# Optimization experiments

Hardware: AMD Instinct MI355X
Metric: run time of the kernel (lower is better)

## Reference

```python
import jax, jax.numpy as jnp
import numpy as np

B, N, I = 8, 1024, 64
E, H, D = 2, 2, 128   # edge types, heads per layer, hidden dim
O = 64                # num_outputs
IN1 = E * H * D       # layer-1 filter input dim (concat of layer-0 heads)


def setup_inputs() -> dict:
    key = jax.random.key(0)
    ks = jax.random.split(key, 20)
    s = lambda f: 1.0 / np.sqrt(f)
    inp = {
        "nodes": jax.random.normal(ks[0], (B, N, I), jnp.float32),
        "edges": jax.random.normal(ks[1], (B, N, N, E), jnp.float32) * 0.1,
        "Wemb": jax.random.normal(ks[2], (I, D), jnp.float32) * s(I),
        "bemb": jnp.zeros((D,), jnp.float32),
        # layer 0 params: filter W, att nets a1/a2 (weight + bias), state bias
        "W0":   jax.random.normal(ks[3], (E, H, D, D), jnp.float32) * s(D),
        "A1w0": jax.random.normal(ks[4], (E, H, D), jnp.float32) * s(D),
        "A1b0": jnp.zeros((E, H), jnp.float32),
        "A2w0": jax.random.normal(ks[5], (E, H, D), jnp.float32) * s(D),
        "A2b0": jnp.zeros((E, H), jnp.float32),
        "SB0":  jnp.zeros((E, H, D), jnp.float32),
        # layer 1 params (input dim = E*H*D from concat)
        "W1":   jax.random.normal(ks[6], (E, H, IN1, D), jnp.float32) * s(IN1),
        "A1w1": jax.random.normal(ks[7], (E, H, D), jnp.float32) * s(D),
        "A1b1": jnp.zeros((E, H), jnp.float32),
        "A2w1": jax.random.normal(ks[8], (E, H, D), jnp.float32) * s(D),
        "A2b1": jnp.zeros((E, H), jnp.float32),
        "SB1":  jnp.zeros((E, H, D), jnp.float32),
        "Wout": jax.random.normal(ks[9], (D, O), jnp.float32) * s(D),
        "bout": jnp.zeros((O,), jnp.float32),
    }
    return inp


def _gat_layer(state, edges_ebnn, W, a1w, a1b, a2w, a2b, sb):
    # state: (B,N,Fin); W: (E,H,Fin,D); edges_ebnn: (E,1,B,N,N)
    Wh = jnp.einsum('bni,ehid->ehbnd', state, W)                    # (E,H,B,N,D)
    s1 = jnp.einsum('ehbnd,ehd->ehbn', Wh, a1w) + a1b[:, :, None, None]
    s2 = jnp.einsum('ehbnd,ehd->ehbn', Wh, a2w) + a2b[:, :, None, None]
    att = s1[..., :, None] + s2[..., None, :]                       # a1_i + a2_j
    att = jax.nn.leaky_relu(att, 0.2) + edges_ebnn                  # edge-type bias
    att = jax.nn.softmax(att, axis=-2)                              # torch dim=1 (over i)
    msg = jnp.einsum('ehbij,ehbjd->ehbid', att, Wh)                 # bmm aggregation
    return msg + sb[:, :, None, None, :]                            # (E,H,B,N,D)


def reference(nodes, edges, Wemb, bemb,
              W0, A1w0, A1b0, A2w0, A2b0, SB0,
              W1, A1w1, A1b1, A2w1, A2b1, SB1,
              Wout, bout):
    edges_e = jnp.transpose(edges, (3, 0, 1, 2))[:, None]           # (E,1,B,N,N)
    state = jax.nn.relu(nodes @ Wemb + bemb)                        # SlimFC embedding
    # layer 0: concat heads/edgetypes along feature dim (torch order jj outer, ii inner)
    m0 = _gat_layer(state, edges_e, W0, A1w0, A1b0, A2w0, A2b0, SB0)
    state = jnp.transpose(m0, (2, 3, 0, 1, 4)).reshape(B, N, E * H * D)
    # layer 1 (last): elu then mean over all heads/edgetypes
    m1 = jax.nn.elu(_gat_layer(state, edges_e, W1, A1w1, A1b1, A2w1, A2b1, SB1))
    state = jnp.mean(m1, axis=(0, 1))                               # (B,N,D)
    return state @ Wout + bout                                      # (B,N,O)
```

## Files before the change

### kernel.cpp

```cpp
#include <hip/hip_runtime.h>
#include <math.h>

#define NB 8
#define NN 1024
#define NI 64
#define EHC 4
#define ND 128
#define NO 64
#define FIN1 512
#define BN 8192
#define LOG2E 1.4426950408889634f

typedef __attribute__((ext_vector_type(8))) short short8;
typedef __attribute__((ext_vector_type(4))) float f32x4;

__device__ __forceinline__ unsigned short f2bf(float f) {
    union { float f; unsigned u; } v; v.f = f;
    unsigned r = v.u + 0x7FFF + ((v.u >> 16) & 1);
    return (unsigned short)(r >> 16);
}
__device__ __forceinline__ unsigned short f2h(float f) {
    union { _Float16 h; unsigned short u; } v;
    v.h = (_Float16)f;
    return v.u;
}
__device__ __forceinline__ float h2f(unsigned short u) {
    union { unsigned short u; _Float16 h; } v;
    v.u = u;
    return (float)v.h;
}

__global__ void prepTk(const float* __restrict__ W0, const float* __restrict__ W1,
                       const float* __restrict__ Wemb, const float* __restrict__ Wout,
                       unsigned short* __restrict__ W0T, unsigned short* __restrict__ W1T,
                       unsigned short* __restrict__ WembT, unsigned short* __restrict__ WoutT) {
    int idx = blockIdx.x * 256 + threadIdx.x;
    if (idx < EHC * ND * ND) {
        int eh = idx >> 14, d = (idx >> 7) & 127, k = idx & 127;
        W0T[idx] = f2bf(W0[((size_t)(eh * ND + k)) * ND + d]);
    }
    int idx1 = idx - EHC * ND * ND;
    if (idx1 >= 0 && idx1 < EHC * ND * FIN1) {
        int eh = idx1 >> 16;
        int r = idx1 & 65535;
        int d = r >> 9, k = r & 511;
        W1T[idx1] = f2bf(W1[((size_t)(eh * FIN1 + k)) * ND + d]);
    }
    int idx2 = idx - (EHC * ND * ND + EHC * ND * FIN1);
    if (idx2 >= 0 && idx2 < ND * NI) {
        int d = idx2 >> 6, k = idx2 & 63;
        WembT[idx2] = f2bf(Wemb[k * ND + d]);
    }
    int idx3 = idx - (EHC * ND * ND + EHC * ND * FIN1 + ND * NI);
    if (idx3 >= 0 && idx3 < ND * NO) {
        int o = idx3 >> 7, d = idx3 & 127;
        WoutT[idx3] = f2bf(Wout[d * NO + o]);
    }
}

__global__ __launch_bounds__(256, 4) void embwh0k(
    const float* __restrict__ nodes, const unsigned short* __restrict__ WembT,
    const float* __restrict__ bemb, const unsigned short* __restrict__ W0T,
    unsigned short* __restrict__ WhT, const float* __restrict__ a1w,
    const float* __restrict__ a1b, const float* __restrict__ a2w,
    const float* __restrict__ a2b, float* __restrict__ s1, float* __restrict__ s2) {
    int id = blockIdx.x;
    int g = id & 7, s_ = id >> 3;
    int eh = s_ & 3;
    int row0 = ((s_ >> 2) * 8 + g) * 32;
    int t = threadIdx.x;
    int w = t >> 6, lane = t & 63;
    int m = lane & 15, quad = lane >> 4;

    __shared__ unsigned short stateL[32 * 136];

    f32x4 accE[2][2];
#pragma unroll
    for (int mt = 0; mt < 2; ++mt)
#pragma unroll
        for (int nt = 0; nt < 2; ++nt) accE[mt][nt] = (f32x4){0.f, 0.f, 0.f, 0.f};
#pragma unroll
    for (int kt = 0; kt < 2; ++kt) {
        short8 aE[2], bE[2];
#pragma unroll
        for (int mt = 0; mt < 2; ++mt) {
            const float* np = nodes + (size_t)(row0 + mt * 16 + m) * NI + kt * 32 + quad * 8;
            f32x4 v0 = *(const f32x4*)np;
            f32x4 v1 = *(const f32x4*)(np + 4);
            union { unsigned short us[8]; short8 s8; } pk;
#pragma unroll
            for (int r = 0; r < 4; ++r) {
                pk.us[r] = f2bf(v0[r]);
                pk.us[r + 4] = f2bf(v1[r]);
            }
            aE[mt] = pk.s8;
        }
#pragma unroll
        for (int nt = 0; nt < 2; ++nt)
            bE[nt] = *(const short8*)(WembT + (w * 32 + nt * 16 + m) * NI + kt * 32 + quad * 8);
#pragma unroll
        for (int mt = 0; mt < 2; ++mt)
#pragma unroll
            for (int nt = 0; nt < 2; ++nt)
                accE[mt][nt] =
                    __builtin_amdgcn_mfma_f32_16x16x32_bf16(aE[mt], bE[nt], accE[mt][nt], 0, 0, 0);
    }
#pragma unroll
    for (int mt = 0; mt < 2; ++mt)
#pragma unroll
        for (int nt = 0; nt < 2; ++nt) {
            int d = w * 32 + nt * 16 + m;
            float bb = bemb[d];
#pragma unroll
            for (int r = 0; r < 4; ++r) {
                float v = fmaxf(accE[mt][nt][r] + bb, 0.f);
                stateL[(mt * 16 + quad * 4 + r) * 136 + d] = f2bf(v);
            }
        }
    __syncthreads();

    f32x4 acc[2][2];
#pragma unroll
    for (int mt = 0; mt < 2; ++mt)
#pragma unroll
        for (int nt = 0; nt < 2; ++nt) acc[mt][nt] = (f32x4){0.f, 0.f, 0.f, 0.f};
#pragma unroll
    for (int k0 = 0; k0 < ND; k0 += 32) {
        short8 a[2], b[2];
#pragma unroll
        for (int mt = 0; mt < 2; ++mt)
            a[mt] = *(const short8*)&stateL[(mt * 16 + m) * 136 + k0 + quad * 8];
#pragma unroll
        for (int nt = 0; nt < 2; ++nt)
            b[nt] = *(const short8*)(W0T + ((size_t)(eh * ND + w * 32 + nt * 16 + m)) * ND +
                                     k0 + quad * 8);
#pragma unroll
        for (int mt = 0; mt < 2; ++mt)
#pragma unroll
            for (int nt = 0; nt < 2; ++nt)
                acc[mt][nt] =
                    __builtin_amdgcn_mfma_f32_16x16x32_bf16(a[mt], b[nt], acc[mt][nt], 0, 0, 0);
    }

    int b_ = row0 >> 10, i0b = row0 & 1023;
    int ehb = eh * NB + b_;
#pragma unroll
    for (int mt = 0; mt < 2; ++mt)
#pragma unroll
        for (int nt = 0; nt < 2; ++nt) {
            int d = w * 32 + nt * 16 + m;
            int i = i0b + mt * 16 + quad * 4;
            union { unsigned short us[4]; unsigned long long u64; } pk;
#pragma unroll
            for (int r = 0; r < 4; ++r) pk.us[r] = f2bf(acc[mt][nt][r]);
            *(unsigned long long*)(WhT + (((size_t)ehb) * ND + d) * NN + i) = pk.u64;
        }
    float w1a = a1w[eh * ND + w * 32 + m], w1b = a1w[eh * ND + w * 32 + 16 + m];
    float w2a = a2w[eh * ND + w * 32 + m], w2b = a2w[eh * ND + w * 32 + 16 + m];
    float p1[2][4], p2[2][4];
#pragma unroll
    for (int mt = 0; mt < 2; ++mt)
#pragma unroll
        for (int r = 0; r < 4; ++r) {
            p1[mt][r] = acc[mt][0][r] * w1a + acc[mt][1][r] * w1b;
            p2[mt][r] = acc[mt][0][r] * w2a + acc[mt][1][r] * w2b;
        }
#pragma unroll
    for (int off = 8; off >= 1; off >>= 1)
#pragma unroll
        for (int mt = 0; mt < 2; ++mt)
#pragma unroll
            for (int r = 0; r < 4; ++r) {
                p1[mt][r] += __shfl_xor(p1[mt][r], off);
                p2[mt][r] += __shfl_xor(p2[mt][r], off);
            }
    __shared__ float sred[2][4][4][8];
    if (m == 0) {
#pragma unroll
        for (int mt = 0; mt < 2; ++mt)
#pragma unroll
            for (int r = 0; r < 4; ++r) {
                sred[0][w][quad][mt * 4 + r] = p1[mt][r];
                sred[1][w][quad][mt * 4 + r] = p2[mt][r];
            }
    }
    __syncthreads();
    if (t < 32) {
        int mt = t >> 4, quad2 = (t >> 2) & 3, r = t & 3;
        int c = mt * 4 + r;
        float v = sred[0][0][quad2][c] + sred[0][1][quad2][c] + sred[0][2][quad2][c] +
                  sred[0][3][quad2][c];
        s1[(size_t)ehb * NN + i0b + t] = (v + a1b[eh]) * LOG2E;
    } else if (t < 64) {
        int tl = t - 32;
        int mt = tl >> 4, quad2 = (tl >> 2) & 3, r = tl & 3;
        int c = mt * 4 + r;
        float v = sred[1][0][quad2][c] + sred[1][1][quad2][c] + sred[1][2][quad2][c] +
                  sred[1][3][quad2][c];
        s2[(size_t)ehb * NN + i0b + tl] = (v + a2b[eh]) * LOG2E;
    }
}

__global__ __launch_bounds__(256, 4) void whgemm1k(
    const unsigned short* __restrict__ state, const unsigned short* __restrict__ WT,
    unsigned short* __restrict__ WhT, const float* __restrict__ a1w,
    const float* __restrict__ a1b, const float* __restrict__ a2w,
    const float* __restrict__ a2b, float* __restrict__ s1, float* __restrict__ s2,
    float* __restrict__ outz) {
    int id = blockIdx.x;
    int g = id & 7, s_ = id >> 3;
    int eh = s_ & 3;
    int row0 = ((s_ >> 2) * 8 + g) * 32;
    int t = threadIdx.x;
    int w = t >> 6, lane = t & 63;
    int m = lane & 15, quad = lane >> 4;

    {
        f32x4 z = (f32x4){0.f, 0.f, 0.f, 0.f};
        for (int idx = t; idx < 128; idx += 256) ((f32x4*)outz)[(size_t)id * 128 + idx] = z;
    }

    f32x4 acc[2][2];
#pragma unroll
    for (int mt = 0; mt < 2; ++mt)
#pragma unroll
        for (int nt = 0; nt < 2; ++nt) acc[mt][nt] = (f32x4){0.f, 0.f, 0.f, 0.f};

    const unsigned short* Ab = state + (size_t)(row0 + m) * FIN1 + quad * 8;
    const unsigned short* Bb = WT + ((size_t)eh * ND + w * 32 + m) * FIN1 + quad * 8;
#pragma unroll 4
    for (int k0 = 0; k0 < FIN1; k0 += 32) {
        short8 a[2], b[2];
#pragma unroll
        for (int mt = 0; mt < 2; ++mt)
            a[mt] = *(const short8*)(Ab + (size_t)mt * 16 * FIN1 + k0);
#pragma unroll
        for (int nt = 0; nt < 2; ++nt)
            b[nt] = *(const short8*)(Bb + (size_t)nt * 16 * FIN1 + k0);
#pragma unroll
        for (int mt = 0; mt < 2; ++mt)
#pragma unroll
            for (int nt = 0; nt < 2; ++nt)
                acc[mt][nt] =
                    __builtin_amdgcn_mfma_f32_16x16x32_bf16(a[mt], b[nt], acc[mt][nt], 0, 0, 0);
    }
    int b_ = row0 >> 10, i0b = row0 & 1023;
    int ehb = eh * NB + b_;
#pragma unroll
    for (int mt = 0; mt < 2; ++mt)
#pragma unroll
        for (int nt = 0; nt < 2; ++nt) {
            int d = w * 32 + nt * 16 + m;
            int i = i0b + mt * 16 + quad * 4;
            union { unsigned short us[4]; unsigned long long u64; } pk;
#pragma unroll
            for (int r = 0; r < 4; ++r) pk.us[r] = f2bf(acc[mt][nt][r]);
            *(unsigned long long*)(WhT + (((size_t)ehb) * ND + d) * NN + i) = pk.u64;
        }
    float w1a = a1w[eh * ND + w * 32 + m], w1b = a1w[eh * ND + w * 32 + 16 + m];
    float w2a = a2w[eh * ND + w * 32 + m], w2b = a2w[eh * ND + w * 32 + 16 + m];
    float p1[2][4], p2[2][4];
#pragma unroll
    for (int mt = 0; mt < 2; ++mt)
#pragma unroll
        for (int r = 0; r < 4; ++r) {
            p1[mt][r] = acc[mt][0][r] * w1a + acc[mt][1][r] * w1b;
            p2[mt][r] = acc[mt][0][r] * w2a + acc[mt][1][r] * w2b;
        }
#pragma unroll
    for (int off = 8; off >= 1; off >>= 1)
#pragma unroll
        for (int mt = 0; mt < 2; ++mt)
#pragma unroll
            for (int r = 0; r < 4; ++r) {
                p1[mt][r] += __shfl_xor(p1[mt][r], off);
                p2[mt][r] += __shfl_xor(p2[mt][r], off);
            }
    __shared__ float sred[2][4][4][8];
    if (m == 0) {
#pragma unroll
        for (int mt = 0; mt < 2; ++mt)
#pragma unroll
            for (int r = 0; r < 4; ++r) {
                sred[0][w][quad][mt * 4 + r] = p1[mt][r];
                sred[1][w][quad][mt * 4 + r] = p2[mt][r];
            }
    }
    __syncthreads();
    if (t < 32) {
        int mt = t >> 4, quad2 = (t >> 2) & 3, r = t & 3;
        int c = mt * 4 + r;
        float v = sred[0][0][quad2][c] + sred[0][1][quad2][c] + sred[0][2][quad2][c] +
                  sred[0][3][quad2][c];
        s1[(size_t)ehb * NN + i0b + t] = (v + a1b[eh]) * LOG2E;
    } else if (t < 64) {
        int tl = t - 32;
        int mt = tl >> 4, quad2 = (tl >> 2) & 3, r = tl & 3;
        int c = mt * 4 + r;
        float v = sred[1][0][quad2][c] + sred[1][1][quad2][c] + sred[1][2][quad2][c] +
                  sred[1][3][quad2][c];
        s2[(size_t)ehb * NN + i0b + tl] = (v + a2b[eh]) * LOG2E;
    }
}

template <int CONV>
__global__ __launch_bounds__(256, 4) void colsumk(const float* __restrict__ edges,
                                                  unsigned short* __restrict__ edgesP,
                                                  const float* __restrict__ s1,
                                                  const float* __restrict__ s2,
                                                  float* __restrict__ Spart) {
    const size_t PO = (size_t)NB * NN * NN;
    int jt = blockIdx.x, b = blockIdx.y, ic = blockIdx.z;
    int t = threadIdx.x;
    int jp = t & 31, is = t >> 5;
    int j = jt * 64 + jp * 2;
    __shared__ float s1L[4][128];
    for (int idx = t; idx < 512; idx += 256) {
        int eh = idx >> 7;
        s1L[eh][idx & 127] = s1[((size_t)eh * NB + b) * NN + ic * 128 + (idx & 127)];
    }
    __syncthreads();
    float s2v[4][2], acc4[4][2];
#pragma unroll
    for (int eh = 0; eh < 4; ++eh) {
        s2v[eh][0] = s2[((size_t)eh * NB + b) * NN + j];
        s2v[eh][1] = s2[((size_t)eh * NB + b) * NN + j + 1];
        acc4[eh][0] = 0.f;
        acc4[eh][1] = 0.f;
    }
    int irow0 = ic * 128 + is * 16;
    const float4* ep = (const float4*)edges + (size_t)(b * NN + irow0) * (NN / 2) + jt * 32 + jp;
    unsigned short* pb = edgesP + (size_t)(b * NN + irow0) * NN + j;
#pragma unroll 4
    for (int ii = 0; ii < 16; ++ii) {
        unsigned q0, q1;
        if (CONV) {
            float4 ev = ep[(size_t)ii * (NN / 2)];
            q0 = (unsigned)f2h(ev.x * LOG2E) | ((unsigned)f2h(ev.z * LOG2E) << 16);
            q1 = (unsigned)f2h(ev.y * LOG2E) | ((unsigned)f2h(ev.w * LOG2E) << 16);
            *(unsigned*)(pb + (size_t)ii * NN) = q0;
            *(unsigned*)(pb + PO + (size_t)ii * NN) = q1;
        } else {
            q0 = *(const unsigned*)(pb + (size_t)ii * NN);
            q1 = *(const unsigned*)(pb + PO + (size_t)ii * NN);
        }
        float p0lo = h2f((unsigned short)(q0 & 0xffff)), p0hi = h2f((unsigned short)(q0 >> 16));
        float p1lo = h2f((unsigned short)(q1 & 0xffff)), p1hi = h2f((unsigned short)(q1 >> 16));
#pragma unroll
        for (int eh = 0; eh < 4; ++eh) {
            float sv = s1L[eh][is * 16 + ii];
            float x0 = sv + s2v[eh][0];
            x0 = fmaxf(x0, 0.2f * x0);
            acc4[eh][0] += __builtin_exp2f(x0 + (eh < 2 ? p0lo : p1lo));
            float x1 = sv + s2v[eh][1];
            x1 = fmaxf(x1, 0.2f * x1);
            acc4[eh][1] += __builtin_exp2f(x1 + (eh < 2 ? p0hi : p1hi));
        }
    }
    __shared__ float red[8][4][64];
#pragma unroll
    for (int eh = 0; eh < 4; ++eh) {
        red[is][eh][jp * 2] = acc4[eh][0];
        red[is][eh][jp * 2 + 1] = acc4[eh][1];
    }
    __syncthreads();
    if (t < 256) {
        int eho = t >> 6, jlo = t & 63;
        float Sv = 0.f;
#pragma unroll
        for (int isx = 0; isx < 8; ++isx) Sv += red[isx][eho][jlo];
        Spart[(((size_t)ic * EHC + eho) * NB + b) * NN + jt * 64 + jlo] = Sv;
    }
}

__global__ __launch_bounds__(256, 2) void msgk(const unsigned short* __restrict__ edgesP,
                                               const unsigned short* __restrict__ WhT,
                                               const float* __restrict__ s1,
                                               const float* __restrict__ s2,
                                               const float* __restrict__ Spart,
                                               const float* __restrict__ sb,
                                               unsigned short* __restrict__ out0,
                                               const unsigned short* __restrict__ WoutT,
                                               const float* __restrict__ bout,
                                               float* __restrict__ out, int mode) {
    int id = blockIdx.x;
    int b = id & 7;
    int s_ = id >> 3;
    int eh = s_ & 3;
    int itile = s_ >> 2;
    int e = eh >> 1;
    int t = threadIdx.x;
    int w = t >> 6, lane = t & 63;
    int n = lane & 15, quad = lane >> 4;
    int dh = w & 1, isub = w >> 1;
    int i0w = itile * 64 + isub * 32;

    __shared__ float2 stL[NN];
    __shared__ unsigned short eluL[2][32][136];

    int base = (eh * NB + b) * NN;
    const size_t pstr = (size_t)EHC * NB * NN;
    for (int jj = t; jj < NN; jj += 256) {
        float S = 0.f;
#pragma unroll
        for (int ic = 0; ic < 8; ++ic) S += Spart[(size_t)ic * pstr + base + jj];
        stL[jj] = make_float2(s2[base + jj], -__builtin_log2f(S));
    }
    float s1r0 = s1[base + i0w + n];
    float s1r1 = s1[base + i0w + 16 + n];
    __syncthreads();

    f32x4 acc[2][4];
#pragma unroll
    for (int bf = 0; bf < 2; ++bf)
#pragma unroll
        for (int dt = 0; dt < 4; ++dt) acc[bf][dt] = (f32x4){0.f, 0.f, 0.f, 0.f};

    const unsigned short* Ap =
        WhT + ((size_t)base * ND + (size_t)(dh * 64 + n) * NN) + quad * 8;
    const unsigned short* Ep =
        edgesP + ((size_t)(e * NB + b) * NN + i0w + n) * NN + quad * 8;

    for (int kc = 0; kc < 32; ++kc) {
        int j0 = kc * 32;
        short8 a[4];
#pragma unroll
        for (int dt = 0; dt < 4; ++dt)
            a[dt] = *(const short8*)(Ap + (size_t)(dt * 16) * NN + j0);
        short8 ev0 = *(const short8*)(Ep + j0);
        short8 ev1 = *(const short8*)(Ep + (size_t)16 * NN + j0);
        float2 stj[8];
#pragma unroll
        for (int r = 0; r < 8; ++r) stj[r] = stL[j0 + quad * 8 + r];
        union { unsigned short us[8]; short8 s8; } pk0, pk1;
#pragma unroll
        for (int r = 0; r < 8; ++r) {
            float x0 = s1r0 + stj[r].x;
            x0 = fmaxf(x0, 0.2f * x0);
            x0 += h2f((unsigned short)ev0[r]) + stj[r].y;
            pk0.us[r] = f2bf(__builtin_exp2f(x0));
            float x1 = s1r1 + stj[r].x;
            x1 = fmaxf(x1, 0.2f * x1);
            x1 += h2f((unsigned short)ev1[r]) + stj[r].y;
            pk1.us[r] = f2bf(__builtin_exp2f(x1));
        }
#pragma unroll
        for (int dt = 0; dt < 4; ++dt) {
            acc[0][dt] = __builtin_amdgcn_mfma_f32_16x16x32_bf16(a[dt], pk0.s8, acc[0][dt], 0, 0, 0);
            acc[1][dt] = __builtin_amdgcn_mfma_f32_16x16x32_bf16(a[dt], pk1.s8, acc[1][dt], 0, 0, 0);
        }
    }

    if (mode == 0) {
#pragma unroll
        for (int bf = 0; bf < 2; ++bf)
#pragma unroll
            for (int dt = 0; dt < 4; ++dt) {
                int d0g = dh * 64 + dt * 16 + quad * 4;
                int i = i0w + bf * 16 + n;
                f32x4 sbv = *(const f32x4*)&sb[eh * ND + d0g];
                union { unsigned short us[4]; unsigned long long u64; } pk;
#pragma unroll
                for (int r = 0; r < 4; ++r) pk.us[r] = f2bf(acc[bf][dt][r] + sbv[r]);
                *(unsigned long long*)(out0 + (size_t)(b * NN + i) * FIN1 + eh * ND + d0g) =
                    pk.u64;
            }
    } else {
#pragma unroll
        for (int bf = 0; bf < 2; ++bf)
#pragma unroll
            for (int dt = 0; dt < 4; ++dt) {
                int dloc = dh * 64 + dt * 16 + quad * 4;
                f32x4 sbv = *(const f32x4*)&sb[eh * ND + dloc];
                union { unsigned short us[4]; unsigned long long u64; } pk;
#pragma unroll
                for (int r = 0; r < 4; ++r) {
                    float v = acc[bf][dt][r] + sbv[r];
                    pk.us[r] = f2bf(v > 0.f ? v : expm1f(v));
                }
                *(unsigned long long*)&eluL[isub][bf * 16 + n][dloc] = pk.u64;
            }
        __syncthreads();
#pragma unroll
        for (int it = 0; it < 2; ++it)
#pragma unroll
            for (int ot = 0; ot < 2; ++ot) {
                int o = (dh * 2 + ot) * 16 + n;
                f32x4 hacc = (f32x4){0.f, 0.f, 0.f, 0.f};
#pragma unroll
                for (int k0 = 0; k0 < 4; ++k0) {
                    short8 av = *(const short8*)&eluL[isub][it * 16 + n][k0 * 32 + quad * 8];
                    short8 bv = *(const short8*)(WoutT + (size_t)o * ND + k0 * 32 + quad * 8);
                    hacc = __builtin_amdgcn_mfma_f32_16x16x32_bf16(av, bv, hacc, 0, 0, 0);
                }
                float bo = bout[o];
                float* op = out + (size_t)(b * NN + i0w + it * 16 + quad * 4) * NO + o;
#pragma unroll
                for (int r = 0; r < 4; ++r)
                    atomicAdd(op + (size_t)r * NO, 0.25f * hacc[r] + 0.25f * bo);
            }
    }
}

extern "C" void kernel_launch(void* const* d_in, const int* in_sizes, int n_in,
                              void* d_out, int out_size, void* d_ws, size_t ws_size,
                              hipStream_t stream) {
    const float* nodes = (const float*)d_in[0];
    const float* edges = (const float*)d_in[1];
    const float* Wemb = (const float*)d_in[2];
    const float* bemb = (const float*)d_in[3];
    const float* W0 = (const float*)d_in[4];
    const float* A1w0 = (const float*)d_in[5];
    const float* A1b0 = (const float*)d_in[6];
    const float* A2w0 = (const float*)d_in[7];
    const float* A2b0 = (const float*)d_in[8];
    const float* SB0 = (const float*)d_in[9];
    const float* W1 = (const float*)d_in[10];
    const float* A1w1 = (const float*)d_in[11];
    const float* A1b1 = (const float*)d_in[12];
    const float* A2w1 = (const float*)d_in[13];
    const float* A2b1 = (const float*)d_in[14];
    const float* SB1 = (const float*)d_in[15];
    const float* Wout = (const float*)d_in[16];
    const float* bout = (const float*)d_in[17];
    float* out = (float*)d_out;

    char* p = (char*)d_ws;
    auto alloc = [&](size_t bytes) {
        char* r = p;
        p += (bytes + 255) & ~(size_t)255;
        return r;
    };
    unsigned short* W0T = (unsigned short*)alloc((size_t)EHC * ND * ND * 2);
    unsigned short* W1T = (unsigned short*)alloc((size_t)EHC * ND * FIN1 * 2);
    unsigned short* WembT = (unsigned short*)alloc((size_t)ND * NI * 2);
    unsigned short* WoutT = (unsigned short*)alloc((size_t)ND * NO * 2);
    unsigned short* WhT = (unsigned short*)alloc((size_t)EHC * BN * ND * 2);
    unsigned short* state1 = (unsigned short*)alloc((size_t)BN * FIN1 * 2);
    float* s1b = (float*)alloc((size_t)EHC * BN * 4);
    float* s2b = (float*)alloc((size_t)EHC * BN * 4);
    float* Spart = (float*)alloc((size_t)8 * EHC * BN * 4);
    unsigned short* edgesP = (unsigned short*)alloc((size_t)2 * NB * NN * NN * 2);

    prepTk<<<1344, 256, 0, stream>>>(W0, W1, Wemb, Wout, W0T, W1T, WembT, WoutT);
    embwh0k<<<1024, 256, 0, stream>>>(nodes, WembT, bemb, W0T, WhT, A1w0, A1b0, A2w0, A2b0,
                                      s1b, s2b);
    colsumk<1><<<dim3(NN / 64, NB, 8), 256, 0, stream>>>(edges, edgesP, s1b, s2b, Spart);
    msgk<<<512, 256, 0, stream>>>(edgesP, WhT, s1b, s2b, Spart, SB0, state1, WoutT, bout,
                                  out, 0);
    whgemm1k<<<1024, 256, 0, stream>>>(state1, W1T, WhT, A1w1, A1b1, A2w1, A2b1, s1b, s2b,
                                       out);
    colsumk<0><<<dim3(NN / 64, NB, 8), 256, 0, stream>>>(edges, edgesP, s1b, s2b, Spart);
    msgk<<<512, 256, 0, stream>>>(edgesP, WhT, s1b, s2b, Spart, SB1, state1, WoutT, bout,
                                  out, 1);
}
```

Baseline: 302.1 us.

## Fold softmax column normalization into Wh and retile msgk per-wave over full D

Adds a small kernel that sums the partial column sums and scales each WhT row in place by 1/S, so msgk no longer reads Spart, takes a log2 or adds the normalizer inside the exp loop. msgk is retiled so each wave covers 16 rows and all 128 feature columns, computing one exp tile per k-step for 8 MFMAs instead of two tiles for 4 each, which halves redundant exp work across waves. The cost is an extra launch plus a read-modify-write of WhT, an extra bf16 rounding of the scaled Wh, and more accumulator registers per wave.

```diff
diff --git a/kernel.cpp b/kernel.cpp
--- a/kernel.cpp
+++ b/kernel.cpp
@@ -13,11 +13,16 @@
 
 typedef __attribute__((ext_vector_type(8))) short short8;
 typedef __attribute__((ext_vector_type(4))) float f32x4;
+typedef __attribute__((ext_vector_type(2))) unsigned uint32x2;
 
 __device__ __forceinline__ unsigned short f2bf(float f) {
     union { float f; unsigned u; } v; v.f = f;
     unsigned r = v.u + 0x7FFF + ((v.u >> 16) & 1);
     return (unsigned short)(r >> 16);
+}
+__device__ __forceinline__ float bf2f(unsigned short u) {
+    union { unsigned u; float f; } v; v.u = (unsigned)u << 16;
+    return v.f;
 }
 __device__ __forceinline__ unsigned short f2h(float f) {
     union { _Float16 h; unsigned short u; } v;
@@ -373,11 +378,37 @@
     }
 }
 
+__global__ __launch_bounds__(256) void whsck(const float* __restrict__ Spart,
+                                             unsigned short* __restrict__ WhT) {
+    int id = blockIdx.x;
+    int ehb = id >> 3, dc = id & 7;
+    int t = threadIdx.x;
+    __shared__ float sinv[NN];
+    const size_t pstr = (size_t)EHC * NB * NN;
+    int base = ehb * NN;
+    for (int jj = t; jj < NN; jj += 256) {
+        float S = 0.f;
+#pragma unroll
+        for (int ic = 0; ic < 8; ++ic) S += Spart[(size_t)ic * pstr + base + jj];
+        sinv[jj] = 1.0f / S;
+    }
+    __syncthreads();
+#pragma unroll 2
+    for (int dr = 0; dr < 16; ++dr) {
+        unsigned short* row = WhT + ((size_t)ehb * ND + dc * 16 + dr) * NN;
+        int jj = t * 4;
+        union { unsigned short us[4]; unsigned long long u64; } v;
+        v.u64 = *(unsigned long long*)(row + jj);
+#pragma unroll
+        for (int k = 0; k < 4; ++k) v.us[k] = f2bf(bf2f(v.us[k]) * sinv[jj + k]);
+        *(unsigned long long*)(row + jj) = v.u64;
+    }
+}
+
 __global__ __launch_bounds__(256, 2) void msgk(const unsigned short* __restrict__ edgesP,
-                                               const unsigned short* __restrict__ WhT,
+                                               const unsigned short* __restrict__ WhS,
                                                const float* __restrict__ s1,
                                                const float* __restrict__ s2,
-                                               const float* __restrict__ Spart,
                                                const float* __restrict__ sb,
                                                unsigned short* __restrict__ out0,
                                                const unsigned short* __restrict__ WoutT,
@@ -392,113 +423,87 @@
     int t = threadIdx.x;
     int w = t >> 6, lane = t & 63;
     int n = lane & 15, quad = lane >> 4;
-    int dh = w & 1, isub = w >> 1;
-    int i0w = itile * 64 + isub * 32;
-
-    __shared__ float2 stL[NN];
-    __shared__ unsigned short eluL[2][32][136];
+    int i0w = itile * 64 + w * 16;
+
+    __shared__ float stL[NN];
+    __shared__ unsigned short eluL[4][16][136];
 
     int base = (eh * NB + b) * NN;
-    const size_t pstr = (size_t)EHC * NB * NN;
-    for (int jj = t; jj < NN; jj += 256) {
-        float S = 0.f;
-#pragma unroll
-        for (int ic = 0; ic < 8; ++ic) S += Spart[(size_t)ic * pstr + base + jj];
-        stL[jj] = make_float2(s2[base + jj], -__builtin_log2f(S));
-    }
-    float s1r0 = s1[base + i0w + n];
-    float s1r1 = s1[base + i0w + 16 + n];
-    __syncthreads();
-
-    f32x4 acc[2][4];
-#pragma unroll
-    for (int bf = 0; bf < 2; ++bf)
-#pragma unroll
-        for (int dt = 0; dt < 4; ++dt) acc[bf][dt] = (f32x4){0.f, 0.f, 0.f, 0.f};
-
-    const unsigned short* Ap =
-        WhT + ((size_t)base * ND + (size_t)(dh * 64 + n) * NN) + quad * 8;
+    for (int jj = t; jj < NN; jj += 256) stL[jj] = s2[base + jj];
+    float s1r = s1[base + i0w + n];
+    __syncthreads();
+
+    f32x4 acc[8];
+#pragma unroll
+    for (int dt = 0; dt < 8; ++dt) acc[dt] = (f32x4){0.f, 0.f, 0.f, 0.f};
+
+    const unsigned short* Ap = WhS + (size_t)base * ND + (size_t)n * NN + quad * 8;
     const unsigned short* Ep =
         edgesP + ((size_t)(e * NB + b) * NN + i0w + n) * NN + quad * 8;
 
+#pragma unroll 2
     for (int kc = 0; kc < 32; ++kc) {
         int j0 = kc * 32;
-        short8 a[4];
-#pragma unroll
-        for (int dt = 0; dt < 4; ++dt)
+        short8 a[8];
+#pragma unroll
+        for (int dt = 0; dt < 8; ++dt)
             a[dt] = *(const short8*)(Ap + (size_t)(dt * 16) * NN + j0);
-        short8 ev0 = *(const short8*)(Ep + j0);
-        short8 ev1 = *(const short8*)(Ep + (size_t)16 * NN + j0);
-        float2 stj[8];
-#pragma unroll
-        for (int r = 0; r < 8; ++r) stj[r] = stL[j0 + quad * 8 + r];
-        union { unsigned short us[8]; short8 s8; } pk0, pk1;
+        short8 ev = *(const short8*)(Ep + j0);
+        f32x4 st0 = *(const f32x4*)&stL[j0 + quad * 8];
+        f32x4 st1 = *(const f32x4*)&stL[j0 + quad * 8 + 4];
+        union { unsigned short us[8]; short8 s8; } pk;
 #pragma unroll
         for (int r = 0; r < 8; ++r) {
-            float x0 = s1r0 + stj[r].x;
-            x0 = fmaxf(x0, 0.2f * x0);
-            x0 += h2f((unsigned short)ev0[r]) + stj[r].y;
-            pk0.us[r] = f2bf(__builtin_exp2f(x0));
-            float x1 = s1r1 + stj[r].x;
-            x1 = fmaxf(x1, 0.2f * x1);
-            x1 += h2f((unsigned short)ev1[r]) + stj[r].y;
-            pk1.us[r] = f2bf(__builtin_exp2f(x1));
-        }
-#pragma unroll
-        for (int dt = 0; dt < 4; ++dt) {
-            acc[0][dt] = __builtin_amdgcn_mfma_f32_16x16x32_bf16(a[dt], pk0.s8, acc[0][dt], 0, 0, 0);
-            acc[1][dt] = __builtin_amdgcn_mfma_f32_16x16x32_bf16(a[dt], pk1.s8, acc[1][dt], 0, 0, 0);
-        }
+            float x = s1r + (r < 4 ? st0[r] : st1[r - 4]);
+            x = fmaxf(x, 0.2f * x);
+            x += h2f((unsigned short)ev[r]);
+            pk.us[r] = f2bf(__builtin_exp2f(x));
+        }
+#pragma unroll
+        for (int dt = 0; dt < 8; ++dt)
+            acc[dt] = __builtin_amdgcn_mfma_f32_16x16x32_bf16(a[dt], pk.s8, acc[dt], 0, 0, 0);
     }
 
     if (mode == 0) {
-#pragma unroll
-        for (int bf = 0; bf < 2; ++bf)
-#pragma unroll
-            for (int dt = 0; dt < 4; ++dt) {
-                int d0g = dh * 64 + dt * 16 + quad * 4;
-                int i = i0w + bf * 16 + n;
-                f32x4 sbv = *(const f32x4*)&sb[eh * ND + d0g];
-                union { unsigned short us[4]; unsigned long long u64; } pk;
-#pragma unroll
-                for (int r = 0; r < 4; ++r) pk.us[r] = f2bf(acc[bf][dt][r] + sbv[r]);
-                *(unsigned long long*)(out0 + (size_t)(b * NN + i) * FIN1 + eh * ND + d0g) =
-                    pk.u64;
-            }
+        int i = i0w + n;
+#pragma unroll
+        for (int dt = 0; dt < 8; ++dt) {
+            int d0g = dt * 16 + quad * 4;
+            f32x4 sbv = *(const f32x4*)&sb[eh * ND + d0g];
+            union { unsigned short us[4]; unsigned long long u64; } pk;
+#pragma unroll
+            for (int r = 0; r < 4; ++r) pk.us[r] = f2bf(acc[dt][r] + sbv[r]);
+            *(unsigned long long*)(out0 + (size_t)(b * NN + i) * FIN1 + eh * ND + d0g) = pk.u64;
+        }
     } else {
 #pragma unroll
-        for (int bf = 0; bf < 2; ++bf)
-#pragma unroll
-            for (int dt = 0; dt < 4; ++dt) {
-                int dloc = dh * 64 + dt * 16 + quad * 4;
-                f32x4 sbv = *(const f32x4*)&sb[eh * ND + dloc];
-                union { unsigned short us[4]; unsigned long long u64; } pk;
-#pragma unroll
-                for (int r = 0; r < 4; ++r) {
-                    float v = acc[bf][dt][r] + sbv[r];
-                    pk.us[r] = f2bf(v > 0.f ? v : expm1f(v));
-                }
-                *(unsigned long long*)&eluL[isub][bf * 16 + n][dloc] = pk.u64;
-            }
-        __syncthreads();
-#pragma unroll
-        for (int it = 0; it < 2; ++it)
-#pragma unroll
-            for (int ot = 0; ot < 2; ++ot) {
-                int o = (dh * 2 + ot) * 16 + n;
-                f32x4 hacc = (f32x4){0.f, 0.f, 0.f, 0.f};
-#pragma unroll
-                for (int k0 = 0; k0 < 4; ++k0) {
-                    short8 av = *(const short8*)&eluL[isub][it * 16 + n][k0 * 32 + quad * 8];
-                    short8 bv = *(const short8*)(WoutT + (size_t)o * ND + k0 * 32 + quad * 8);
-                    hacc = __builtin_amdgcn_mfma_f32_16x16x32_bf16(av, bv, hacc, 0, 0, 0);
-                }
-                float bo = bout[o];
-                float* op = out + (size_t)(b * NN + i0w + it * 16 + quad * 4) * NO + o;
-#pragma unroll
-                for (int r = 0; r < 4; ++r)
-                    atomicAdd(op + (size_t)r * NO, 0.25f * hacc[r] + 0.25f * bo);
-            }
+        for (int dt = 0; dt < 8; ++dt) {
+            int d0g = dt * 16 + quad * 4;
+            f32x4 sbv = *(const f32x4*)&sb[eh * ND + d0g];
+            union { unsigned short us[4]; unsigned long long u64; } pk;
+#pragma unroll
+            for (int r = 0; r < 4; ++r) {
+                float v = acc[dt][r] + sbv[r];
+                pk.us[r] = f2bf(v > 0.f ? v : expm1f(v));
+            }
+            *(unsigned long long*)&eluL[w][n][d0g] = pk.u64;
+        }
+#pragma unroll
+        for (int ot = 0; ot < 4; ++ot) {
+            int o = ot * 16 + n;
+            f32x4 hacc = (f32x4){0.f, 0.f, 0.f, 0.f};
+#pragma unroll
+            for (int k0 = 0; k0 < 4; ++k0) {
+                short8 av = *(const short8*)&eluL[w][n][k0 * 32 + quad * 8];
+                short8 bv = *(const short8*)(WoutT + (size_t)o * ND + k0 * 32 + quad * 8);
+                hacc = __builtin_amdgcn_mfma_f32_16x16x32_bf16(av, bv, hacc, 0, 0, 0);
+            }
+            float bo = bout[o];
+            float* op = out + (size_t)(b * NN + i0w + quad * 4) * NO + o;
+#pragma unroll
+            for (int r = 0; r < 4; ++r)
+                atomicAdd(op + (size_t)r * NO, 0.25f * hacc[r] + 0.25f * bo);
+        }
     }
 }
 
@@ -546,11 +551,11 @@
     embwh0k<<<1024, 256, 0, stream>>>(nodes, WembT, bemb, W0T, WhT, A1w0, A1b0, A2w0, A2b0,
                                       s1b, s2b);
     colsumk<1><<<dim3(NN / 64, NB, 8), 256, 0, stream>>>(edges, edgesP, s1b, s2b, Spart);
-    msgk<<<512, 256, 0, stream>>>(edgesP, WhT, s1b, s2b, Spart, SB0, state1, WoutT, bout,
-                                  out, 0);
+    whsck<<<256, 256, 0, stream>>>(Spart, WhT);
+    msgk<<<512, 256, 0, stream>>>(edgesP, WhT, s1b, s2b, SB0, state1, WoutT, bout, out, 0);
     whgemm1k<<<1024, 256, 0, stream>>>(state1, W1T, WhT, A1w1, A1b1, A2w1, A2b1, s1b, s2b,
                                        out);
     colsumk<0><<<dim3(NN / 64, NB, 8), 256, 0, stream>>>(edges, edgesP, s1b, s2b, Spart);
-    msgk<<<512, 256, 0, stream>>>(edgesP, WhT, s1b, s2b, Spart, SB1, state1, WoutT, bout,
-                                  out, 1);
-}
+    whsck<<<256, 256, 0, stream>>>(Spart, WhT);
+    msgk<<<512, 256, 0, stream>>>(edgesP, WhT, s1b, s2b, SB1, state1, WoutT, bout, out, 1);
+}
```

After: 354.6 us. +17.4%, slower.
